# Kernel tuning notes

Hardware: AMD Instinct MI355X
Metric: run time of the kernel (lower is better)

Reference implementation:

```python
import jax, jax.numpy as jnp
import numpy as np

BASE_RES = 192          # image_shape = [192, 192]
VIEWS = 128             # radial views
READOUT_OS = 2.0        # readout oversampling
SAMPLES = int(BASE_RES * READOUT_OS)  # 384 samples per spoke


def _radial_traj_and_weights():
    """Linear-ordered full-range 2D radial trajectory + ramp density weights."""
    t = jnp.arange(SAMPLES, dtype=jnp.float32)
    # radius spans [-pi, pi) along each spoke (NUFFT convention)
    r = (t - SAMPLES / 2) / (SAMPLES / 2) * jnp.pi            # [samples]
    theta = jnp.arange(VIEWS, dtype=jnp.float32) * (jnp.pi / VIEWS)  # [views]
    kx = r[None, :] * jnp.cos(theta)[:, None]                 # [views, samples]
    ky = r[None, :] * jnp.sin(theta)[:, None]
    points = jnp.stack([kx, ky], axis=-1).reshape(-1, 2)      # [M, 2]
    # geometric (ramp) density compensation: weight ~ |k| with DC floor
    rho = jnp.abs(r) / jnp.pi                                 # [samples], in [0, 1]
    w = jnp.maximum(rho, 1.0 / SAMPLES)                       # avoid zero at DC
    weights = jnp.broadcast_to(w[None, :], (VIEWS, SAMPLES)).reshape(-1)  # [M]
    return points, weights


def setup_inputs() -> dict:
    key = jax.random.key(0)
    x = jax.random.normal(key, (2, BASE_RES, BASE_RES, 2), dtype=jnp.float32)
    points, weights = _radial_traj_and_weights()
    return {"x": x, "points": points, "weights": weights}


def _nudft_resample(xc, points, weights):
    """Type-2 NUDFT (forward) -> density comp -> type-1 NUDFT (adjoint).

    xc: complex [C, B, H, W]; points: [M, 2] in [-pi, pi); weights: [M].
    The 2D nonuniform DFT phase factorizes per axis: exp(-i(kx*nx + ky*ny)).
    """
    C, B, H, W = xc.shape
    nx = (jnp.arange(H, dtype=jnp.float32) - H // 2)          # grid indices
    ny = (jnp.arange(W, dtype=jnp.float32) - W // 2)
    Ax = jnp.exp(-1j * (points[:, 0:1] * nx[None, :]).astype(jnp.complex64))  # [M, H]
    Ay = jnp.exp(-1j * (points[:, 1:2] * ny[None, :]).astype(jnp.complex64))  # [M, W]
    # type-2: k[m] = sum_{h,w} x[h,w] exp(-i(kx_m h + ky_m w))
    tmp = jnp.einsum('cbhw,mh->cbmw', xc, Ax)                 # [C, B, M, W]
    k = jnp.einsum('cbmw,mw->cbm', tmp, Ay)                   # [C, B, M]
    # density compensation
    k = k * weights.astype(jnp.complex64)
    # type-1 adjoint: img[h,w] = sum_m k[m] exp(+i(kx_m h + ky_m w))
    tmp2 = jnp.einsum('cbm,mh->cbmh', k, jnp.conj(Ax))        # [C, B, M, H]
    img = jnp.einsum('cbmh,mw->cbhw', tmp2, jnp.conj(Ay))     # [C, B, H, W]
    # scale by 1 / num_elements(image_shape)
    return img / jnp.asarray(H * W, dtype=jnp.complex64)


def reference(x, points, weights):
    # inputs [B, H, W, C] -> channels-first [C, B, H, W] (layer's perm)
    rank = x.ndim
    perm = [rank - 1] + list(range(rank - 1))
    xc = jnp.transpose(x, perm).astype(jnp.complex64)
    img = _nudft_resample(xc, points, weights)
    out = jnp.abs(img)                                        # layer dtype is real
    inv_perm = list(range(1, rank)) + [0]
    return jnp.transpose(out, inv_perm)                       # [B, H, W, C]
```

## Files before the change

### kernel.cpp

```cpp
#include <hip/hip_runtime.h>
#include <math.h>


#define HH 192
#define WW 192
#define NVIEWS 128
#define NSAMP 384
#define NPIX (HH*WW)
#define HALFT 193
#define M2 12545
#define M2P 12672
#define KTOT 25344
#define NSPLITK 33

typedef __attribute__((ext_vector_type(8))) short bf16x8;
typedef __attribute__((ext_vector_type(4))) float f32x4;
typedef __attribute__((ext_vector_type(8))) unsigned short u16x8;

__device__ __forceinline__ void rot(float& cr, float& ci, float dr, float di) {
  float nr = cr*dr - ci*di;
  float ni = cr*di + ci*dr;
  cr = nr; ci = ni;
}
__device__ __forceinline__ unsigned short f2b(float f) {
  unsigned int u = __float_as_uint(f);
  u += 0x7fffu + ((u >> 16) & 1u);
  return (unsigned short)(u >> 16);
}
__device__ __forceinline__ float b2f(unsigned short h) {
  return __uint_as_float(((unsigned int)h) << 16);
}

__global__ __launch_bounds__(256) void phase_kernel(
    const float* __restrict__ points, const float* __restrict__ x,
    unsigned short* __restrict__ BT, unsigned short* __restrict__ CxT,
    unsigned short* __restrict__ SxT, unsigned short* __restrict__ Am,
    unsigned short* __restrict__ XT, float* __restrict__ kyv) {
  const int v2 = blockIdx.x;
  const int role = blockIdx.y;
  const int t = threadIdx.x;
  if (role == 8) {
    for (int idx = v2*256 + t; idx < 768*192; idx += 65*256) {
      const int n = idx / 192, h = idx - n*192;
      const int cb = n / 192, w = n - cb*192;
      const int b = cb >> 1, c = cb & 1;
      XT[idx] = f2b(x[(((size_t)b*HH + h)*WW + w)*2 + c]);
    }
    for (int idx = v2*256 + t; idx < M2P; idx += 65*256) {
      if (idx < M2) {
        const int v2b = idx / HALFT, tb = idx - v2b*HALFT;
        kyv[idx] = points[(v2b*NSAMP + tb)*2 + 1];
      } else {
        kyv[idx] = 0.f;
      }
    }
    return;
  }
  if (t >= HALFT) return;
  if (role < 4) {
    const int hsplit = role;
    const float kx = points[(v2*NSAMP + t)*2 + 0];
    const int m2 = v2*HALFT + t;
    const int h0 = hsplit*48;
    float cr, ci; __sincosf(kx*(float)(h0-96), &ci, &cr);
    float dr, di; __sincosf(kx, &di, &dr);
    u16x8 pc, ps;
    for (int j = 0; j < 48; ++j) {
      const int h = h0 + j;
      CxT[(size_t)h*M2P + m2] = f2b(cr);
      SxT[(size_t)h*M2P + m2] = f2b(ci);
      pc[j&7] = f2b(cr); ps[j&7] = f2b(ci);
      if ((j&7) == 7) {
        *(u16x8*)(Am + (size_t)m2*192 + (h-7))         = pc;
        *(u16x8*)(Am + (size_t)(12672+m2)*192 + (h-7)) = ps;
      }
      rot(cr, ci, dr, di);
    }
  } else {
    const int wsplit = role - 4;
    const float ky = points[(v2*NSAMP + t)*2 + 1];
    const int kap = v2*HALFT + t;
    const int w0 = wsplit*48;
    float cr, ci; __sincosf(ky*(float)(w0-96), &ci, &cr);
    float dr, di; __sincosf(ky, &di, &dr);
    for (int j = 0; j < 48; ++j) {
      BT[(size_t)(w0+j)*KTOT + kap]       = f2b(cr);
      BT[(size_t)(w0+j)*KTOT + M2P + kap] = f2b(ci);
      rot(cr, ci, dr, di);
    }
  }
}


__global__ __launch_bounds__(256) void gemm1_kernel(
    const unsigned short* __restrict__ Am, const unsigned short* __restrict__ XT,
    const float* __restrict__ kyv, float* __restrict__ Abuf) {
  __shared__ float lds[2][128][2];
  const int L = blockIdx.x;
  const int idx0 = (L & 7)*99 + (L >> 3);
  const int mt = idx0 >> 2;
  const int cb = idx0 & 3;
  const int wv = threadIdx.x >> 6;
  const int lane = threadIdx.x & 63;
  const int r = lane & 15, kg = lane >> 4;
  const int mhalf = wv >> 1;
  const int whalf = wv & 1;
  const int mbase = mt*128 + mhalf*64;
  const int wbase = whalf*96;
  const int nbase = cb*192 + wbase;

  f32x4 acc[4][6];
  #pragma unroll
  for (int a = 0; a < 4; ++a)
    #pragma unroll
    for (int b = 0; b < 6; ++b) acc[a][b] = (f32x4){0.f,0.f,0.f,0.f};

  const unsigned short* Ap = Am + (size_t)(mbase + r)*192 + kg*8;
  const unsigned short* Bp = XT + (size_t)(nbase + r)*192 + kg*8;
  #pragma unroll
  for (int ks = 0; ks < 6; ++ks) {
    bf16x8 af[4], bfr[6];
    #pragma unroll
    for (int mf = 0; mf < 4; ++mf)
      af[mf] = *(const bf16x8*)(Ap + (size_t)mf*16*192 + ks*32);
    #pragma unroll
    for (int nf = 0; nf < 6; ++nf)
      bfr[nf] = *(const bf16x8*)(Bp + (size_t)nf*16*192 + ks*32);
    #pragma unroll
    for (int mf = 0; mf < 4; ++mf)
      #pragma unroll
      for (int nf = 0; nf < 6; ++nf)
        acc[mf][nf] = __builtin_amdgcn_mfma_f32_16x16x32_bf16(
            af[mf], bfr[nf], acc[mf][nf], 0, 0, 0);
  }

  const bool isCx = (mt < 99);
  const int m2w = mbase - (isCx ? 0 : 12672);
  float accA[16], accB[16];
  #pragma unroll
  for (int mf = 0; mf < 4; ++mf)
    #pragma unroll
    for (int reg = 0; reg < 4; ++reg) {
      const int m2 = m2w + mf*16 + kg*4 + reg;
      const float ky = kyv[m2];
      float a0 = 0.f, b0 = 0.f;
      #pragma unroll
      for (int nf = 0; nf < 6; ++nf) {
        const float wo = (float)(wbase + nf*16 + r - 96);
        float sy, cy; __sincosf(ky*wo, &sy, &cy);
        const float g = acc[mf][nf][reg];
        a0 = fmaf(g, cy, a0);
        b0 = fmaf(g, sy, b0);
      }
      accA[mf*4+reg] = a0; accB[mf*4+reg] = b0;
    }
  #pragma unroll
  for (int msk = 1; msk <= 8; msk <<= 1) {
    #pragma unroll
    for (int i = 0; i < 16; ++i) {
      accA[i] += __shfl_xor(accA[i], msk);
      accB[i] += __shfl_xor(accB[i], msk);
    }
  }
  if (r == 0) {
    #pragma unroll
    for (int mf = 0; mf < 4; ++mf)
      #pragma unroll
      for (int reg = 0; reg < 4; ++reg) {
        const int mloc = mhalf*64 + mf*16 + kg*4 + reg;
        lds[whalf][mloc][0] = accA[mf*4+reg];
        lds[whalf][mloc][1] = accB[mf*4+reg];
      }
  }
  __syncthreads();
  {
    const int tid = threadIdx.x;
    const int mloc = tid >> 1, slot = tid & 1;
    const float val = lds[0][mloc][slot] + lds[1][mloc][slot];
    const int m2 = mt*128 + mloc - (isCx ? 0 : 12672);
    const int oidx = isCx ? (slot ? 3 : 0) : (slot ? 1 : 2);
    Abuf[((size_t)cb*M2P + m2)*4 + oidx] = val;
  }
}


__global__ __launch_bounds__(256) void tmat_kernel(
    const float* __restrict__ Abuf, const float* __restrict__ weights,
    const unsigned short* __restrict__ CxT, const unsigned short* __restrict__ SxT,
    unsigned short* __restrict__ A, float* __restrict__ K2edge) {
  const int m2 = blockIdx.x*256 + threadIdx.x;
  if (m2 >= M2P) return;
  const int role = blockIdx.y;
  if (role == 192) {
    if (m2 >= M2) return;
    const int v2 = m2 / HALFT, t = m2 - v2*HALFT;
    if (t != 0 && t != 192) return;
    const float f = weights[t] * (1.0f/36864.0f);
    const bool hp = (v2 >= 1 && v2 <= 63);
    const int d = (t == 0) ? 0 : 1;
    #pragma unroll
    for (int cb = 0; cb < 4; ++cb) {
      const float4 Av = *(const float4*)(Abuf + ((size_t)cb*M2P + m2)*4);
      const float A1 = Av.x, A2 = Av.y, A3 = Av.z, A4 = Av.w;
      float* e = K2edge + ((v2*2 + d)*4 + cb)*2;
      e[0] = f*(A1 - A2); e[1] = -f*(A3 + A4);
      if (hp) {
        float* e2 = K2edge + (((128 - v2)*2 + d)*4 + cb)*2;
        e2[0] = f*(A1 + A2); e2[1] = f*(A3 - A4);
      }
    }
    return;
  }
  const int h = role;
  if (m2 >= M2) {
    #pragma unroll
    for (int cb = 0; cb < 4; ++cb) {
      unsigned short* Arow = A + (size_t)(cb*192 + h)*KTOT;
      Arow[m2] = 0; Arow[M2P + m2] = 0;
    }
    return;
  }
  const int v2 = m2 / HALFT, t = m2 - v2*HALFT;
  float f = weights[t] * (1.0f/36864.0f);
  if (t != 0 && t != 192) f *= 2.0f;
  const bool hp = (v2 >= 1 && v2 <= 63);
  const float cx = b2f(CxT[(size_t)h*M2P + m2]);
  const float sx = b2f(SxT[(size_t)h*M2P + m2]);
  #pragma unroll
  for (int cb = 0; cb < 4; ++cb) {
    const float4 Av = *(const float4*)(Abuf + ((size_t)cb*M2P + m2)*4);
    const float A1 = Av.x, A2 = Av.y, A3 = Av.z, A4 = Av.w;
    float p0, p1, q0, q1;
    if (hp) {
      p0 = 2.f*f*A1; p1 = 2.f*f*A3; q0 = 2.f*f*A4; q1 = 2.f*f*A2;
    } else {
      const float kr = f*(A1 - A2), ki = -f*(A3 + A4);
      p0 = kr; p1 = -ki; q0 = -ki; q1 = -kr;
    }
    unsigned short* Arow = A + (size_t)(cb*192 + h)*KTOT;
    Arow[m2]       = f2b(p0*cx + p1*sx);
    Arow[M2P + m2] = f2b(q0*cx + q1*sx);
  }
}

__global__ __launch_bounds__(256) void adj_gemm(
    const unsigned short* __restrict__ A, const unsigned short* __restrict__ BT,
    unsigned short* __restrict__ partials) {
  const int L = blockIdx.x;
  const int xcd = L & 7, slot = L >> 3;
  const int g = slot / 6;
  const int kc = g*8 + xcd;
  if (kc >= NSPLITK) return;
  const int mt = slot - g*6;
  const int wv = threadIdx.x >> 6;
  const int lane = threadIdx.x & 63;
  const int r = lane & 15, kg = lane >> 4;
  const int jbase = mt*128 + (wv>>1)*64;
  const int wbase = (wv&1)*96;
  const int kb = kc*768 + kg*8;

  f32x4 acc[4][6];
  #pragma unroll
  for (int a = 0; a < 4; ++a)
    #pragma unroll
    for (int b = 0; b < 6; ++b) acc[a][b] = (f32x4){0.f,0.f,0.f,0.f};

  const unsigned short* Ap = A + (size_t)(jbase + r)*KTOT + kb;
  const unsigned short* Bp = BT + (size_t)(wbase + r)*KTOT + kb;
  for (int ks = 0; ks < 24; ++ks) {
    bf16x8 af[4], bfr[6];
    #pragma unroll
    for (int mf = 0; mf < 4; ++mf)
      af[mf] = *(const bf16x8*)(Ap + (size_t)mf*16*KTOT + ks*32);
    #pragma unroll
    for (int nf = 0; nf < 6; ++nf)
      bfr[nf] = *(const bf16x8*)(Bp + (size_t)nf*16*KTOT + ks*32);
    #pragma unroll
    for (int mf = 0; mf < 4; ++mf)
      #pragma unroll
      for (int nf = 0; nf < 6; ++nf)
        acc[mf][nf] = __builtin_amdgcn_mfma_f32_16x16x32_bf16(
            af[mf], bfr[nf], acc[mf][nf], 0, 0, 0);
  }
  unsigned short* base = partials + (size_t)kc*147456;
  #pragma unroll
  for (int mf = 0; mf < 4; ++mf)
    #pragma unroll
    for (int nf = 0; nf < 6; ++nf) {
      const int w = wbase + nf*16 + r;
      const int j = jbase + mf*16 + kg*4;
      ushort4 u = make_ushort4(f2b(acc[mf][nf][0]), f2b(acc[mf][nf][1]),
                               f2b(acc[mf][nf][2]), f2b(acc[mf][nf][3]));
      *(ushort4*)(base + (size_t)w*768 + j) = u;
    }
}

__global__ __launch_bounds__(256) void finish_kernel(
    const unsigned short* __restrict__ BT, const unsigned short* __restrict__ CxT,
    const unsigned short* __restrict__ SxT, const float* __restrict__ K2edge,
    const unsigned short* __restrict__ partials, float* __restrict__ out) {
  __shared__ float cxs[65][8], sxs[65][8], cys[65][8], sys[65][8];
  __shared__ float redI[4][64][4], redR[4][64][4];
  const int bx = blockIdx.x;
  const int h0 = (bx/24)*8, w0 = (bx%24)*8;
  const int tid = threadIdx.x;
  for (int i = tid; i < 65*8; i += 256) {
    const int v2 = i >> 3, e = i & 7;
    const int kap = v2*HALFT;
    cxs[v2][e] = b2f(CxT[(size_t)(h0+e)*M2P + kap]);
    sxs[v2][e] = b2f(SxT[(size_t)(h0+e)*M2P + kap]);
    cys[v2][e] = b2f(BT[(size_t)(w0+e)*KTOT + kap]);
    sys[v2][e] = b2f(BT[(size_t)(w0+e)*KTOT + M2P + kap]);
  }
  __syncthreads();
  const int g = tid >> 6, hi = (tid >> 3) & 7, wi = tid & 7;
  const int h = h0 + hi, w = w0 + wi;
  float im[4] = {0,0,0,0};
  for (int v = g*32; v < g*32 + 32; ++v) {
    const int v2 = (v <= 64) ? v : 128 - v;
    const float sg = (v <= 64) ? 1.f : -1.f;
    const float cx = cxs[v2][hi], sx = sg*sxs[v2][hi];
    const float cy = cys[v2][wi], sy = sys[v2][wi];
    const float t1 = cx*sy + sx*cy;
    const float t2 = cx*cy - sx*sy;
    const int idx = v*16;
    #pragma unroll
    for (int cb = 0; cb < 4; ++cb)
      im[cb] += K2edge[idx + cb*2]*t1 + K2edge[idx + cb*2 + 1]*t2;
  }
  float re[4] = {0,0,0,0};
  for (int kc = g; kc < NSPLITK; kc += 4) {
    const unsigned short* p = partials + (size_t)kc*147456 + (size_t)w*768;
    #pragma unroll
    for (int cb = 0; cb < 4; ++cb)
      re[cb] += b2f(p[cb*192 + h]);
  }
  const int p = tid & 63;
  #pragma unroll
  for (int cb = 0; cb < 4; ++cb) { redI[g][p][cb] = im[cb]; redR[g][p][cb] = re[cb]; }
  __syncthreads();
  if (g == 0) {
    #pragma unroll
    for (int cb = 0; cb < 4; ++cb) {
      im[cb] += redI[1][p][cb] + redI[2][p][cb] + redI[3][p][cb];
      re[cb] += redR[1][p][cb] + redR[2][p][cb] + redR[3][p][cb];
    }
    const int pix = h*192 + w;
    #pragma unroll
    for (int b = 0; b < 2; ++b)
      #pragma unroll
      for (int c = 0; c < 2; ++c) {
        const int cb = b*2 + c;
        out[((size_t)b*NPIX + pix)*2 + c] = sqrtf(re[cb]*re[cb] + im[cb]*im[cb]);
      }
  }
}


template <int HPER>
__global__ __launch_bounds__(192) void fwd_kernel(
    const float* __restrict__ x, const float* __restrict__ points,
    float* __restrict__ kpart) {
  const int v = blockIdx.x;
  const int split = blockIdx.y;
  const int t = threadIdx.x;
  const int m = v*NSAMP + t;
  const float kx = points[2*m+0];
  const float ky = points[2*m+1];
  const int h0 = split*HPER;

  float kr[4] = {0,0,0,0}, ki[4] = {0,0,0,0};
  float cyr, cyi; __sincosf(96.0f*ky, &cyi, &cyr);
  float dyr, dyi; __sincosf(-ky, &dyi, &dyr);
  float cx0r, cx0i; __sincosf(kx*(float)(96-h0), &cx0i, &cx0r);
  float dxr, dxi; __sincosf(-kx, &dxi, &dxr);

  for (int wp = 0; wp < 96; ++wp) {
    const int w0 = wp*2;
    float g0r[4]={0,0,0,0}, g0i[4]={0,0,0,0};
    float g1r[4]={0,0,0,0}, g1i[4]={0,0,0,0};
    float cxr = cx0r, cxi = cx0i;
    const float* p0 = x + (h0*WW + w0)*2;
    const float* p1 = p0 + HH*WW*2;
    #pragma unroll 4
    for (int h = 0; h < HPER; ++h) {
      float4 a = *(const float4*)(p0 + h*(WW*2));
      float4 b = *(const float4*)(p1 + h*(WW*2));
      g0r[0] += a.x*cxr; g0i[0] += a.x*cxi;
      g0r[1] += a.y*cxr; g0i[1] += a.y*cxi;
      g1r[0] += a.z*cxr; g1i[0] += a.z*cxi;
      g1r[1] += a.w*cxr; g1i[1] += a.w*cxi;
      g0r[2] += b.x*cxr; g0i[2] += b.x*cxi;
      g0r[3] += b.y*cxr; g0i[3] += b.y*cxi;
      g1r[2] += b.z*cxr; g1i[2] += b.z*cxi;
      g1r[3] += b.w*cxr; g1i[3] += b.w*cxi;
      rot(cxr, cxi, dxr, dxi);
    }
    #pragma unroll
    for (int cb = 0; cb < 4; ++cb) {
      kr[cb] += g0r[cb]*cyr - g0i[cb]*cyi;
      ki[cb] += g0r[cb]*cyi + g0i[cb]*cyr;
    }
    rot(cyr, cyi, dyr, dyi);
    #pragma unroll
    for (int cb = 0; cb < 4; ++cb) {
      kr[cb] += g1r[cb]*cyr - g1i[cb]*cyi;
      ki[cb] += g1r[cb]*cyi + g1i[cb]*cyr;
    }
    rot(cyr, cyi, dyr, dyi);
  }
  float* o = kpart + (((split*NVIEWS + v)*192 + t)*4)*2;
  #pragma unroll
  for (int cb = 0; cb < 4; ++cb) { o[2*cb] = kr[cb]; o[2*cb+1] = ki[cb]; }
}

__global__ __launch_bounds__(256) void dc_kernel(
    const float* __restrict__ x, float* __restrict__ dcsum) {
  const int tid = threadIdx.x;
  float s0=0.f, s1=0.f, s2=0.f, s3=0.f;
  for (int i = tid; i < NPIX; i += 256) {
    float2 a = *(const float2*)(x + i*2);
    float2 b = *(const float2*)(x + HH*WW*2 + i*2);
    s0 += a.x; s1 += a.y; s2 += b.x; s3 += b.y;
  }
  #pragma unroll
  for (int off = 32; off > 0; off >>= 1) {
    s0 += __shfl_down(s0, off);
    s1 += __shfl_down(s1, off);
    s2 += __shfl_down(s2, off);
    s3 += __shfl_down(s3, off);
  }
  __shared__ float red[4][4];
  const int wv = tid >> 6, ln = tid & 63;
  if (ln == 0) { red[0][wv]=s0; red[1][wv]=s1; red[2][wv]=s2; red[3][wv]=s3; }
  __syncthreads();
  if (tid < 4) {
    float tot = red[tid][0]+red[tid][1]+red[tid][2]+red[tid][3];
    dcsum[2*tid] = tot; dcsum[2*tid+1] = 0.0f;
  }
}

__global__ __launch_bounds__(256) void combine_kernel(
    const float* __restrict__ kpart, const float* __restrict__ dcsum,
    const float* __restrict__ weights, float* __restrict__ K2, int nsplit) {
  const int idx = blockIdx.x*256 + threadIdx.x;
  if (idx >= NVIEWS*HALFT) return;
  const int v = idx / HALFT, t = idx % HALFT;
  float f = weights[t] * (1.0f/36864.0f);
  if (t != 0 && t != 192) f *= 2.0f;
  float o[8];
  if (t == 192) {
    #pragma unroll
    for (int cb = 0; cb < 4; ++cb) { o[2*cb] = f*dcsum[2*cb]; o[2*cb+1] = f*dcsum[2*cb+1]; }
  } else {
    #pragma unroll
    for (int cb = 0; cb < 4; ++cb) {
      float ar = 0.f, ai = 0.f;
      for (int s = 0; s < nsplit; ++s) {
        const float* p = kpart + (((s*NVIEWS + v)*192 + t)*4 + cb)*2;
        ar += p[0]; ai += p[1];
      }
      o[2*cb] = f*ar; o[2*cb+1] = f*ai;
    }
  }
  float* q = K2 + idx*8;
  #pragma unroll
  for (int j = 0; j < 8; ++j) q[j] = o[j];
}

template <int VPC>
__global__ __launch_bounds__(256) void adj_kernel(
    const float* __restrict__ K2, const float* __restrict__ points,
    float* __restrict__ imgpart) {
  const int pix = blockIdx.x*256 + threadIdx.x;
  const int chunk = blockIdx.y;
  const float nh = (float)(pix / WW - 96);
  const float nw = (float)(pix % WW - 96);
  float re[4] = {0,0,0,0}, im[4] = {0,0,0,0};
  const float INVPI = 0.3183098861837907f;
  const float PI192 = 3.14159265358979f / 192.0f;
  for (int v = chunk*VPC; v < chunk*VPC + VPC; ++v) {
    const float ct = -points[2*(v*NSAMP)+0] * INVPI;
    const float st = -points[2*(v*NSAMP)+1] * INVPI;
    const float alpha = ct*nh + st*nw;
    const float delta = alpha * PI192;
    float dr, di; __sincosf(delta, &di, &dr);
    float c0r, c0i; __sincosf(-192.0f*delta, &c0i, &c0r);
    const float* Kv = K2 + v*HALFT*8;
    #pragma unroll
    for (int cb = 0; cb < 4; ++cb) {
      float a = Kv[2*cb], b = Kv[2*cb+1];
      re[cb] += a*c0r - b*c0i;
      im[cb] += a*c0i + b*c0r;
    }
    float d2r = dr*dr - di*di, d2i = 2.0f*dr*di;
    float ar = c0r*dr - c0i*di, ai = c0r*di + c0i*dr;
    float br = ar*dr - ai*di,  bi = ar*di + ai*dr;
    for (int i = 0; i < 95; ++i) {
      const float* ka = Kv + (2*i+1)*8;
      const float* kb = Kv + (2*i+2)*8;
      #pragma unroll
      for (int cb = 0; cb < 4; ++cb)
        re[cb] += ka[2*cb]*ar - ka[2*cb+1]*ai;
      #pragma unroll
      for (int cb = 0; cb < 4; ++cb)
        re[cb] += kb[2*cb]*br - kb[2*cb+1]*bi;
      rot(ar, ai, d2r, d2i);
      rot(br, bi, d2r, d2i);
    }
    {
      const float* ka = Kv + 191*8;
      #pragma unroll
      for (int cb = 0; cb < 4; ++cb)
        re[cb] += ka[2*cb]*ar - ka[2*cb+1]*ai;
    }
    const float* kd = Kv + 192*8;
    #pragma unroll
    for (int cb = 0; cb < 4; ++cb) { re[cb] += kd[2*cb]; im[cb] += kd[2*cb+1]; }
  }
  float* o = imgpart + (chunk*NPIX + pix)*8;
  #pragma unroll
  for (int cb = 0; cb < 4; ++cb) { o[2*cb] = re[cb]; o[2*cb+1] = im[cb]; }
}

__global__ __launch_bounds__(256) void out_fb_kernel(
    const float* __restrict__ imgpart, float* __restrict__ out, int nchunk) {
  const int pix = blockIdx.x*256 + threadIdx.x;
  float re[4] = {0,0,0,0}, im[4] = {0,0,0,0};
  for (int ch = 0; ch < nchunk; ++ch) {
    const float* p = imgpart + (ch*NPIX + pix)*8;
    #pragma unroll
    for (int cb = 0; cb < 4; ++cb) { re[cb] += p[2*cb]; im[cb] += p[2*cb+1]; }
  }
  #pragma unroll
  for (int b = 0; b < 2; ++b)
    #pragma unroll
    for (int c = 0; c < 2; ++c) {
      const int cb = b*2 + c;
      out[(b*NPIX + pix)*2 + c] = sqrtf(re[cb]*re[cb] + im[cb]*im[cb]);
    }
}

extern "C" void kernel_launch(void* const* d_in, const int* in_sizes, int n_in,
                              void* d_out, int out_size, void* d_ws, size_t ws_size,
                              hipStream_t stream) {
  const float* x       = (const float*)d_in[0];
  const float* points  = (const float*)d_in[1];
  const float* weights = (const float*)d_in[2];
  float* out = (float*)d_out;

  const size_t OFF_S   = 20334080ull;
  const size_t SZ_AADJ = 38928384ull;
  const size_t NEED    = OFF_S + SZ_AADJ + 9732096ull;

  if (ws_size >= NEED) {
    char* wsb = (char*)d_ws;
    unsigned short* BT   = (unsigned short*)(wsb + 0);
    unsigned short* CxT  = (unsigned short*)(wsb + 9732096);
    unsigned short* SxT  = (unsigned short*)(wsb + 14598144);
    float* K2edge        = (float*)(wsb + 19464192);
    float* kyv           = (float*)(wsb + 19472384);
    float* Abuf          = (float*)(wsb + 19523072);
    char* S              = wsb + OFF_S;
    unsigned short* Am   = (unsigned short*)(S + 0);
    unsigned short* XT   = (unsigned short*)(S + 9732096);
    unsigned short* Aadj = (unsigned short*)(S + 0);
    unsigned short* partials = (unsigned short*)(S + SZ_AADJ);

    phase_kernel<<<dim3(65,9), 256, 0, stream>>>(points, x, BT, CxT, SxT, Am, XT, kyv);
    gemm1_kernel<<<792, 256, 0, stream>>>(Am, XT, kyv, Abuf);
    tmat_kernel<<<dim3((M2P + 255)/256, 193), 256, 0, stream>>>(
        Abuf, weights, CxT, SxT, Aadj, K2edge);
    adj_gemm<<<240, 256, 0, stream>>>(Aadj, BT, partials);
    finish_kernel<<<576, 256, 0, stream>>>(BT, CxT, SxT, K2edge, partials, out);
  } else {
    float* ws = (float*)d_ws;
    const size_t ws_floats = ws_size / sizeof(float);
    int nsplit = 16, nchunk = 16;
    auto need = [&](int ns, int nc) -> size_t {
      return (size_t)ns*196608 + 8 + 197632 + (size_t)nc*294912;
    };
    while (need(nsplit, nchunk) > ws_floats && nchunk > 1) nchunk >>= 1;
    while (need(nsplit, nchunk) > ws_floats && nsplit > 1) nsplit >>= 1;

    float* kpart   = ws;
    float* dcsum   = kpart + (size_t)nsplit*196608;
    float* K2      = dcsum + 8;
    float* imgpart = K2 + 197632;

    switch (nsplit) {
      case 16: fwd_kernel<12><<<dim3(NVIEWS,16), 192, 0, stream>>>(x, points, kpart); break;
      case 8:  fwd_kernel<24><<<dim3(NVIEWS,8),  192, 0, stream>>>(x, points, kpart); break;
      case 4:  fwd_kernel<48><<<dim3(NVIEWS,4),  192, 0, stream>>>(x, points, kpart); break;
      case 2:  fwd_kernel<96><<<dim3(NVIEWS,2),  192, 0, stream>>>(x, points, kpart); break;
      default: fwd_kernel<192><<<dim3(NVIEWS,1), 192, 0, stream>>>(x, points, kpart); break;
    }
    dc_kernel<<<1, 256, 0, stream>>>(x, dcsum);
    combine_kernel<<<(NVIEWS*HALFT + 255)/256, 256, 0, stream>>>(
        kpart, dcsum, weights, K2, nsplit);
    switch (nchunk) {
      case 16: adj_kernel<8>  <<<dim3(NPIX/256,16), 256, 0, stream>>>(K2, points, imgpart); break;
      case 8:  adj_kernel<16> <<<dim3(NPIX/256,8),  256, 0, stream>>>(K2, points, imgpart); break;
      case 4:  adj_kernel<32> <<<dim3(NPIX/256,4),  256, 0, stream>>>(K2, points, imgpart); break;
      case 2:  adj_kernel<64> <<<dim3(NPIX/256,2),  256, 0, stream>>>(K2, points, imgpart); break;
      default: adj_kernel<128><<<dim3(NPIX/256,1),  256, 0, stream>>>(K2, points, imgpart); break;
    }
    out_fb_kernel<<<NPIX/256, 256, 0, stream>>>(imgpart, out, nchunk);
  }
}
```

Before: 123.7 us.

## Fuse five-stage pipeline into one cooperative persistent kernel with grid syncs

Merges the phase, forward GEMM, T-matrix, adjoint GEMM and finish kernels into a single cooperatively launched persistent kernel. The stages are separated by grid-wide syncs instead of separate launches, and each stage loops over its work items with a grid-stride loop. The aim is to remove launch overhead and inter-kernel gaps. In exchange, the grid is capped at the co-resident block count, so occupancy is limited by the union of all stages' register and LDS use. Each grid.sync also adds its own cost. The original five-launch path remains as a fallback when the cooperative launch fails.

```diff
diff --git a/kernel.cpp b/kernel.cpp
--- a/kernel.cpp
+++ b/kernel.cpp
@@ -1,4 +1,5 @@
 #include <hip/hip_runtime.h>
+#include <hip/hip_cooperative_groups.h>
 #include <math.h>
 
 
@@ -30,6 +31,340 @@
 __device__ __forceinline__ float b2f(unsigned short h) {
   return __uint_as_float(((unsigned int)h) << 16);
 }
+
+__global__ void __launch_bounds__(256) mega_kernel(
+    const float* __restrict__ points, const float* __restrict__ x,
+    const float* __restrict__ weights,
+    unsigned short* __restrict__ BT, unsigned short* __restrict__ CxT,
+    unsigned short* __restrict__ SxT, unsigned short* __restrict__ Am,
+    unsigned short* __restrict__ XT, float* __restrict__ kyv,
+    float* __restrict__ Abuf, unsigned short* __restrict__ Aadj,
+    float* __restrict__ K2edge, unsigned short* __restrict__ partials,
+    float* __restrict__ out) {
+  cooperative_groups::grid_group grid = cooperative_groups::this_grid();
+  const int G = gridDim.x;
+  const int bid = blockIdx.x;
+  const int tid = threadIdx.x;
+
+  __shared__ float lds1[2][128][2];
+  __shared__ float cxs[65][8], sxs[65][8], cys[65][8], sys[65][8];
+  __shared__ float redI[4][64][4], redR[4][64][4];
+
+  for (int u = bid; u < 585; u += G) {
+    const int v2 = u % 65;
+    const int role = u / 65;
+    if (role == 8) {
+      for (int idx = v2*256 + tid; idx < 768*192; idx += 65*256) {
+        const int n = idx / 192, h = idx - n*192;
+        const int cb = n / 192, w = n - cb*192;
+        const int b = cb >> 1, c = cb & 1;
+        XT[idx] = f2b(x[(((size_t)b*HH + h)*WW + w)*2 + c]);
+      }
+      for (int idx = v2*256 + tid; idx < M2P; idx += 65*256) {
+        if (idx < M2) {
+          const int v2b = idx / HALFT, tb = idx - v2b*HALFT;
+          kyv[idx] = points[(v2b*NSAMP + tb)*2 + 1];
+        } else {
+          kyv[idx] = 0.f;
+        }
+      }
+    } else if (tid < HALFT) {
+      if (role < 4) {
+        const int hsplit = role;
+        const float kx = points[(v2*NSAMP + tid)*2 + 0];
+        const int m2 = v2*HALFT + tid;
+        const int h0 = hsplit*48;
+        float cr, ci; __sincosf(kx*(float)(h0-96), &ci, &cr);
+        float dr, di; __sincosf(kx, &di, &dr);
+        u16x8 pc, ps;
+        for (int j = 0; j < 48; ++j) {
+          const int h = h0 + j;
+          CxT[(size_t)h*M2P + m2] = f2b(cr);
+          SxT[(size_t)h*M2P + m2] = f2b(ci);
+          pc[j&7] = f2b(cr); ps[j&7] = f2b(ci);
+          if ((j&7) == 7) {
+            *(u16x8*)(Am + (size_t)m2*192 + (h-7))         = pc;
+            *(u16x8*)(Am + (size_t)(12672+m2)*192 + (h-7)) = ps;
+          }
+          rot(cr, ci, dr, di);
+        }
+      } else {
+        const int wsplit = role - 4;
+        const float ky = points[(v2*NSAMP + tid)*2 + 1];
+        const int kap = v2*HALFT + tid;
+        const int w0 = wsplit*48;
+        float cr, ci; __sincosf(ky*(float)(w0-96), &ci, &cr);
+        float dr, di; __sincosf(ky, &di, &dr);
+        for (int j = 0; j < 48; ++j) {
+          BT[(size_t)(w0+j)*KTOT + kap]       = f2b(cr);
+          BT[(size_t)(w0+j)*KTOT + M2P + kap] = f2b(ci);
+          rot(cr, ci, dr, di);
+        }
+      }
+    }
+  }
+  __threadfence();
+  grid.sync();
+
+  for (int L = bid; L < 792; L += G) {
+    const int idx0 = (L & 7)*99 + (L >> 3);
+    const int mt = idx0 >> 2;
+    const int cb = idx0 & 3;
+    const int wv = tid >> 6;
+    const int lane = tid & 63;
+    const int r = lane & 15, kg = lane >> 4;
+    const int mhalf = wv >> 1;
+    const int whalf = wv & 1;
+    const int mbase = mt*128 + mhalf*64;
+    const int wbase = whalf*96;
+    const int nbase = cb*192 + wbase;
+
+    f32x4 acc[4][6];
+    #pragma unroll
+    for (int a = 0; a < 4; ++a)
+      #pragma unroll
+      for (int b = 0; b < 6; ++b) acc[a][b] = (f32x4){0.f,0.f,0.f,0.f};
+
+    const unsigned short* Ap = Am + (size_t)(mbase + r)*192 + kg*8;
+    const unsigned short* Bp = XT + (size_t)(nbase + r)*192 + kg*8;
+    #pragma unroll
+    for (int ks = 0; ks < 6; ++ks) {
+      bf16x8 af[4], bfr[6];
+      #pragma unroll
+      for (int mf = 0; mf < 4; ++mf)
+        af[mf] = *(const bf16x8*)(Ap + (size_t)mf*16*192 + ks*32);
+      #pragma unroll
+      for (int nf = 0; nf < 6; ++nf)
+        bfr[nf] = *(const bf16x8*)(Bp + (size_t)nf*16*192 + ks*32);
+      #pragma unroll
+      for (int mf = 0; mf < 4; ++mf)
+        #pragma unroll
+        for (int nf = 0; nf < 6; ++nf)
+          acc[mf][nf] = __builtin_amdgcn_mfma_f32_16x16x32_bf16(
+              af[mf], bfr[nf], acc[mf][nf], 0, 0, 0);
+    }
+
+    const bool isCx = (mt < 99);
+    const int m2w = mbase - (isCx ? 0 : 12672);
+    float accA[16], accB[16];
+    #pragma unroll
+    for (int mf = 0; mf < 4; ++mf)
+      #pragma unroll
+      for (int reg = 0; reg < 4; ++reg) {
+        const int m2 = m2w + mf*16 + kg*4 + reg;
+        const float ky = kyv[m2];
+        float a0 = 0.f, b0 = 0.f;
+        #pragma unroll
+        for (int nf = 0; nf < 6; ++nf) {
+          const float wo = (float)(wbase + nf*16 + r - 96);
+          float sy, cy; __sincosf(ky*wo, &sy, &cy);
+          const float g = acc[mf][nf][reg];
+          a0 = fmaf(g, cy, a0);
+          b0 = fmaf(g, sy, b0);
+        }
+        accA[mf*4+reg] = a0; accB[mf*4+reg] = b0;
+      }
+    #pragma unroll
+    for (int msk = 1; msk <= 8; msk <<= 1) {
+      #pragma unroll
+      for (int i = 0; i < 16; ++i) {
+        accA[i] += __shfl_xor(accA[i], msk);
+        accB[i] += __shfl_xor(accB[i], msk);
+      }
+    }
+    if (r == 0) {
+      #pragma unroll
+      for (int mf = 0; mf < 4; ++mf)
+        #pragma unroll
+        for (int reg = 0; reg < 4; ++reg) {
+          const int mloc = mhalf*64 + mf*16 + kg*4 + reg;
+          lds1[whalf][mloc][0] = accA[mf*4+reg];
+          lds1[whalf][mloc][1] = accB[mf*4+reg];
+        }
+    }
+    __syncthreads();
+    {
+      const int mloc = tid >> 1, slot = tid & 1;
+      const float val = lds1[0][mloc][slot] + lds1[1][mloc][slot];
+      const int m2 = mt*128 + mloc - (isCx ? 0 : 12672);
+      const int oidx = isCx ? (slot ? 3 : 0) : (slot ? 1 : 2);
+      Abuf[((size_t)cb*M2P + m2)*4 + oidx] = val;
+    }
+    __syncthreads();
+  }
+  __threadfence();
+  grid.sync();
+
+  for (int u = bid; u < 50*193; u += G) {
+    const int mb = u % 50;
+    const int role = u / 50;
+    const int m2 = mb*256 + tid;
+    if (m2 < M2P) {
+      if (role == 192) {
+        if (m2 < M2) {
+          const int v2 = m2 / HALFT, t = m2 - v2*HALFT;
+          if (t == 0 || t == 192) {
+            const float f = weights[t] * (1.0f/36864.0f);
+            const bool hp = (v2 >= 1 && v2 <= 63);
+            const int d = (t == 0) ? 0 : 1;
+            #pragma unroll
+            for (int cb = 0; cb < 4; ++cb) {
+              const float4 Av = *(const float4*)(Abuf + ((size_t)cb*M2P + m2)*4);
+              const float A1 = Av.x, A2 = Av.y, A3 = Av.z, A4 = Av.w;
+              float* e = K2edge + ((v2*2 + d)*4 + cb)*2;
+              e[0] = f*(A1 - A2); e[1] = -f*(A3 + A4);
+              if (hp) {
+                float* e2 = K2edge + (((128 - v2)*2 + d)*4 + cb)*2;
+                e2[0] = f*(A1 + A2); e2[1] = f*(A3 - A4);
+              }
+            }
+          }
+        }
+      } else {
+        const int h = role;
+        if (m2 >= M2) {
+          #pragma unroll
+          for (int cb = 0; cb < 4; ++cb) {
+            unsigned short* Arow = Aadj + (size_t)(cb*192 + h)*KTOT;
+            Arow[m2] = 0; Arow[M2P + m2] = 0;
+          }
+        } else {
+          const int v2 = m2 / HALFT, t = m2 - v2*HALFT;
+          float f = weights[t] * (1.0f/36864.0f);
+          if (t != 0 && t != 192) f *= 2.0f;
+          const bool hp = (v2 >= 1 && v2 <= 63);
+          const float cx = b2f(CxT[(size_t)h*M2P + m2]);
+          const float sx = b2f(SxT[(size_t)h*M2P + m2]);
+          #pragma unroll
+          for (int cb = 0; cb < 4; ++cb) {
+            const float4 Av = *(const float4*)(Abuf + ((size_t)cb*M2P + m2)*4);
+            const float A1 = Av.x, A2 = Av.y, A3 = Av.z, A4 = Av.w;
+            float p0, p1, q0, q1;
+            if (hp) {
+              p0 = 2.f*f*A1; p1 = 2.f*f*A3; q0 = 2.f*f*A4; q1 = 2.f*f*A2;
+            } else {
+              const float kr = f*(A1 - A2), ki = -f*(A3 + A4);
+              p0 = kr; p1 = -ki; q0 = -ki; q1 = -kr;
+            }
+            unsigned short* Arow = Aadj + (size_t)(cb*192 + h)*KTOT;
+            Arow[m2]       = f2b(p0*cx + p1*sx);
+            Arow[M2P + m2] = f2b(q0*cx + q1*sx);
+          }
+        }
+      }
+    }
+  }
+  __threadfence();
+  grid.sync();
+
+  for (int L = bid; L < 240; L += G) {
+    const int xcd = L & 7, slot = L >> 3;
+    const int g = slot / 6;
+    const int kc = g*8 + xcd;
+    if (kc < NSPLITK) {
+      const int mt = slot - g*6;
+      const int wv = tid >> 6;
+      const int lane = tid & 63;
+      const int r = lane & 15, kg = lane >> 4;
+      const int jbase = mt*128 + (wv>>1)*64;
+      const int wbase = (wv&1)*96;
+      const int kb = kc*768 + kg*8;
+
+      f32x4 acc[4][6];
+      #pragma unroll
+      for (int a = 0; a < 4; ++a)
+        #pragma unroll
+        for (int b = 0; b < 6; ++b) acc[a][b] = (f32x4){0.f,0.f,0.f,0.f};
+
+      const unsigned short* Ap = Aadj + (size_t)(jbase + r)*KTOT + kb;
+      const unsigned short* Bp = BT + (size_t)(wbase + r)*KTOT + kb;
+      for (int ks = 0; ks < 24; ++ks) {
+        bf16x8 af[4], bfr[6];
+        #pragma unroll
+        for (int mf = 0; mf < 4; ++mf)
+          af[mf] = *(const bf16x8*)(Ap + (size_t)mf*16*KTOT + ks*32);
+        #pragma unroll
+        for (int nf = 0; nf < 6; ++nf)
+          bfr[nf] = *(const bf16x8*)(Bp + (size_t)nf*16*KTOT + ks*32);
+        #pragma unroll
+        for (int mf = 0; mf < 4; ++mf)
+          #pragma unroll
+          for (int nf = 0; nf < 6; ++nf)
+            acc[mf][nf] = __builtin_amdgcn_mfma_f32_16x16x32_bf16(
+                af[mf], bfr[nf], acc[mf][nf], 0, 0, 0);
+      }
+      unsigned short* base = partials + (size_t)kc*147456;
+      #pragma unroll
+      for (int mf = 0; mf < 4; ++mf)
+        #pragma unroll
+        for (int nf = 0; nf < 6; ++nf) {
+          const int w = wbase + nf*16 + r;
+          const int j = jbase + mf*16 + kg*4;
+          ushort4 uu = make_ushort4(f2b(acc[mf][nf][0]), f2b(acc[mf][nf][1]),
+                                    f2b(acc[mf][nf][2]), f2b(acc[mf][nf][3]));
+          *(ushort4*)(base + (size_t)w*768 + j) = uu;
+        }
+    }
+  }
+  __threadfence();
+  grid.sync();
+
+  for (int u = bid; u < 576; u += G) {
+    const int h0 = (u/24)*8, w0 = (u%24)*8;
+    for (int i = tid; i < 65*8; i += 256) {
+      const int v2 = i >> 3, e = i & 7;
+      const int kap = v2*HALFT;
+      cxs[v2][e] = b2f(CxT[(size_t)(h0+e)*M2P + kap]);
+      sxs[v2][e] = b2f(SxT[(size_t)(h0+e)*M2P + kap]);
+      cys[v2][e] = b2f(BT[(size_t)(w0+e)*KTOT + kap]);
+      sys[v2][e] = b2f(BT[(size_t)(w0+e)*KTOT + M2P + kap]);
+    }
+    __syncthreads();
+    const int g = tid >> 6, hi = (tid >> 3) & 7, wi = tid & 7;
+    const int h = h0 + hi, w = w0 + wi;
+    float im[4] = {0,0,0,0};
+    for (int v = g*32; v < g*32 + 32; ++v) {
+      const int v2 = (v <= 64) ? v : 128 - v;
+      const float sg = (v <= 64) ? 1.f : -1.f;
+      const float cx = cxs[v2][hi], sx = sg*sxs[v2][hi];
+      const float cy = cys[v2][wi], sy = sys[v2][wi];
+      const float t1 = cx*sy + sx*cy;
+      const float t2 = cx*cy - sx*sy;
+      const int idx = v*16;
+      #pragma unroll
+      for (int cb = 0; cb < 4; ++cb)
+        im[cb] += K2edge[idx + cb*2]*t1 + K2edge[idx + cb*2 + 1]*t2;
+    }
+    float re[4] = {0,0,0,0};
+    for (int kc = g; kc < NSPLITK; kc += 4) {
+      const unsigned short* p = partials + (size_t)kc*147456 + (size_t)w*768;
+      #pragma unroll
+      for (int cb = 0; cb < 4; ++cb)
+        re[cb] += b2f(p[cb*192 + h]);
+    }
+    const int p = tid & 63;
+    #pragma unroll
+    for (int cb = 0; cb < 4; ++cb) { redI[g][p][cb] = im[cb]; redR[g][p][cb] = re[cb]; }
+    __syncthreads();
+    if (g == 0) {
+      #pragma unroll
+      for (int cb = 0; cb < 4; ++cb) {
+        im[cb] += redI[1][p][cb] + redI[2][p][cb] + redI[3][p][cb];
+        re[cb] += redR[1][p][cb] + redR[2][p][cb] + redR[3][p][cb];
+      }
+      const int pix = h*192 + w;
+      #pragma unroll
+      for (int b = 0; b < 2; ++b)
+        #pragma unroll
+        for (int c = 0; c < 2; ++c) {
+          const int cb = b*2 + c;
+          out[((size_t)b*NPIX + pix)*2 + c] = sqrtf(re[cb]*re[cb] + im[cb]*im[cb]);
+        }
+    }
+    __syncthreads();
+  }
+}
+
 
 __global__ __launch_bounds__(256) void phase_kernel(
     const float* __restrict__ points, const float* __restrict__ x,
@@ -91,7 +426,6 @@
   }
 }
 
-
 __global__ __launch_bounds__(256) void gemm1_kernel(
     const unsigned short* __restrict__ Am, const unsigned short* __restrict__ XT,
     const float* __restrict__ kyv, float* __restrict__ Abuf) {
@@ -182,7 +516,6 @@
     Abuf[((size_t)cb*M2P + m2)*4 + oidx] = val;
   }
 }
-
 
 __global__ __launch_bounds__(256) void tmat_kernel(
     const float* __restrict__ Abuf, const float* __restrict__ weights,
@@ -567,12 +900,37 @@
     unsigned short* Aadj = (unsigned short*)(S + 0);
     unsigned short* partials = (unsigned short*)(S + SZ_AADJ);
 
-    phase_kernel<<<dim3(65,9), 256, 0, stream>>>(points, x, BT, CxT, SxT, Am, XT, kyv);
-    gemm1_kernel<<<792, 256, 0, stream>>>(Am, XT, kyv, Abuf);
-    tmat_kernel<<<dim3((M2P + 255)/256, 193), 256, 0, stream>>>(
-        Abuf, weights, CxT, SxT, Aadj, K2edge);
-    adj_gemm<<<240, 256, 0, stream>>>(Aadj, BT, partials);
-    finish_kernel<<<576, 256, 0, stream>>>(BT, CxT, SxT, K2edge, partials, out);
+    hipError_t cerr = hipErrorUnknown;
+    int dev = 0;
+    if (hipGetDevice(&dev) == hipSuccess) {
+      hipDeviceProp_t prop;
+      if (hipGetDeviceProperties(&prop, dev) == hipSuccess &&
+          prop.cooperativeLaunch) {
+        int maxB = 0;
+        if (hipOccupancyMaxActiveBlocksPerMultiprocessor(
+                &maxB, mega_kernel, 256, 0) == hipSuccess && maxB > 0) {
+          int G = maxB * prop.multiProcessorCount;
+          if (G > 768) G = 768;
+          if (G >= 64) {
+            void* kargs[] = {
+              (void*)&points, (void*)&x, (void*)&weights,
+              (void*)&BT, (void*)&CxT, (void*)&SxT, (void*)&Am, (void*)&XT,
+              (void*)&kyv, (void*)&Abuf, (void*)&Aadj, (void*)&K2edge,
+              (void*)&partials, (void*)&out};
+            cerr = hipLaunchCooperativeKernel(mega_kernel, dim3(G), dim3(256),
+                                              kargs, 0, stream);
+          }
+        }
+      }
+    }
+    if (cerr != hipSuccess) {
+      phase_kernel<<<dim3(65,9), 256, 0, stream>>>(points, x, BT, CxT, SxT, Am, XT, kyv);
+      gemm1_kernel<<<792, 256, 0, stream>>>(Am, XT, kyv, Abuf);
+      tmat_kernel<<<dim3((M2P + 255)/256, 193), 256, 0, stream>>>(
+          Abuf, weights, CxT, SxT, Aadj, K2edge);
+      adj_gemm<<<240, 256, 0, stream>>>(Aadj, BT, partials);
+      finish_kernel<<<576, 256, 0, stream>>>(BT, CxT, SxT, K2edge, partials, out);
+    }
   } else {
     float* ws = (float*)d_ws;
     const size_t ws_floats = ws_size / sizeof(float);
```

New measurement: 123.6 us. No clear change (-0.1%).
